# Optimization experiments

Hardware: AMD Instinct MI355X
Metric: run time of the kernel (lower is better)

Reference implementation:

```python
import jax, jax.numpy as jnp
import numpy as np

B, S, D_IN, H, D_OUT = 128, 2048, 256, 256, 256
FORECAST = 1

def setup_inputs() -> dict:
    key = jax.random.key(0)
    ks = jax.random.split(key, 20)
    def lin(k, o, i):
        bound = 1.0 / np.sqrt(i)
        return jax.random.uniform(k, (o, i), jnp.float32, -bound, bound)
    def bias(k, o, i):
        bound = 1.0 / np.sqrt(i)
        return jax.random.uniform(k, (o,), jnp.float32, -bound, bound)
    inp = {
        "x": jax.random.normal(ks[0], (B, S, D_IN), jnp.float32),
        # layer 0 (input_size -> hidden)
        "Wf0": lin(ks[1], H, D_IN), "bf0": bias(ks[2], H, D_IN), "Uf0": lin(ks[3], H, H),
        "Wi0": lin(ks[4], H, D_IN), "bi0": bias(ks[5], H, D_IN), "Ui0": lin(ks[6], H, H),
        "Wx0": lin(ks[7], H, D_IN), "bx0": bias(ks[8], H, D_IN),
        # layer 1 (hidden -> hidden)
        "Wf1": lin(ks[9], H, H), "bf1": bias(ks[10], H, H), "Uf1": lin(ks[11], H, H),
        "Wi1": lin(ks[12], H, H), "bi1": bias(ks[13], H, H), "Ui1": lin(ks[14], H, H),
        "Wx1": lin(ks[15], H, H), "bx1": bias(ks[16], H, H),
        # output head
        "fcW": lin(ks[17], D_OUT, H), "fcb": bias(ks[18], D_OUT, H),
    }
    return inp

def _ran_layer(xseq, Wf, bf, Uf, Wi, bi, Ui, Wx, bx):
    # xseq: [B, S, D]. Precompute all input projections in three batched GEMMs,
    # then scan only the recurrent part (h @ U.T + gates + elementwise update).
    xf = jnp.einsum('bsd,hd->bsh', xseq, Wf) + bf  # [B,S,H]
    xi = jnp.einsum('bsd,hd->bsh', xseq, Wi) + bi
    xp = jnp.einsum('bsd,hd->bsh', xseq, Wx) + bx
    def step(h, inp):
        xf_t, xi_t, xp_t = inp                      # each [B,H]
        f = jax.nn.sigmoid(xf_t + h @ Uf.T)
        i = jax.nn.sigmoid(xi_t + h @ Ui.T)
        h = f * h + i * xp_t
        return h, h
    h0 = jnp.zeros((xseq.shape[0], Uf.shape[0]), xseq.dtype)
    seq = (jnp.swapaxes(xf, 0, 1), jnp.swapaxes(xi, 0, 1), jnp.swapaxes(xp, 0, 1))
    _, hs = jax.lax.scan(step, h0, seq)             # hs: [S,B,H]
    return jnp.swapaxes(hs, 0, 1)                   # [B,S,H]

def reference(x, Wf0, bf0, Uf0, Wi0, bi0, Ui0, Wx0, bx0,
              Wf1, bf1, Uf1, Wi1, bi1, Ui1, Wx1, bx1, fcW, fcb):
    h1 = _ran_layer(x,  Wf0, bf0, Uf0, Wi0, bi0, Ui0, Wx0, bx0)
    h2 = _ran_layer(h1, Wf1, bf1, Uf1, Wi1, bi1, Ui1, Wx1, bx1)
    # dropout in eval mode == identity; take last FORECAST steps then fc
    out = h2[:, -FORECAST:, :]                      # [B,FORECAST,H]
    return jnp.einsum('bth,oh->bto', out, fcW) + fcb
```

## Files before the change

kernel.cpp:

```cpp
#include <hip/hip_runtime.h>
#include <hip/hip_bf16.h>
#include <cstdint>
#include <cstddef>


typedef __bf16 bf16;
typedef __bf16 bf16x8 __attribute__((ext_vector_type(8)));
typedef __bf16 bf16x4 __attribute__((ext_vector_type(4)));
typedef __bf16 bf16x2 __attribute__((ext_vector_type(2)));
typedef float  floatx4 __attribute__((ext_vector_type(4)));

#define B_   128
#define S_   2048
#define H_   256
#define NEG_LOG2E -1.442695040888963f
#define NGB  96
#define SMEM_BYTES (84 * 1024)

__global__ void prep_weights(
    const float* __restrict__ Wf0, const float* __restrict__ Wi0, const float* __restrict__ Wx0,
    const float* __restrict__ Wf1, const float* __restrict__ Wi1, const float* __restrict__ Wx1,
    const float* __restrict__ Uf0, const float* __restrict__ Ui0,
    const float* __restrict__ Uf1, const float* __restrict__ Ui1,
    const float* __restrict__ bf0, const float* __restrict__ bi0, const float* __restrict__ bx0,
    const float* __restrict__ bf1, const float* __restrict__ bi1, const float* __restrict__ bx1,
    const float* __restrict__ fcW,
    bf16* __restrict__ W0cat, bf16* __restrict__ W1cat,
    bf16* __restrict__ U0cat, bf16* __restrict__ U1cat,
    float* __restrict__ b0cat, float* __restrict__ b1cat, float* __restrict__ fcWT)
{
    int tid = blockIdx.x * blockDim.x + threadIdx.x;
    int nth = gridDim.x * blockDim.x;
    for (int idx = tid; idx < 768 * 256; idx += nth) {
        int r = idx >> 8, k = idx & 255, rr = r & 255;
        const float* s0 = (r < 256) ? Wf0 : ((r < 512) ? Wi0 : Wx0);
        const float* s1 = (r < 256) ? Wf1 : ((r < 512) ? Wi1 : Wx1);
        W0cat[idx] = (bf16)s0[rr * 256 + k];
        W1cat[idx] = (bf16)s1[rr * 256 + k];
    }
    for (int idx = tid; idx < 512 * 256; idx += nth) {
        int r = idx >> 8, k = idx & 255, rr = r & 255;
        U0cat[idx] = (bf16)((r < 256 ? Uf0 : Ui0)[rr * 256 + k]);
        U1cat[idx] = (bf16)((r < 256 ? Uf1 : Ui1)[rr * 256 + k]);
    }
    for (int idx = tid; idx < 768; idx += nth) {
        const float* s0 = (idx < 256) ? bf0 : ((idx < 512) ? bi0 : bx0);
        const float* s1 = (idx < 256) ? bf1 : ((idx < 512) ? bi1 : bx1);
        b0cat[idx] = s0[idx & 255];
        b1cat[idx] = s1[idx & 255];
    }
    for (int idx = tid; idx < 256 * 256; idx += nth) {
        int h = idx >> 8, o = idx & 255;
        fcWT[idx] = fcW[o * 256 + h];
    }
}

__global__ void convert_x(const float* __restrict__ x, bf16* __restrict__ xa, int t0, int T)
{
    int tid = blockIdx.x * blockDim.x + threadIdx.x;
    int d4 = tid & 63;
    int b  = (tid >> 6) & 127;
    int t  = tid >> 13;
    if (t >= T) return;
    const float4* src = (const float4*)(x + ((size_t)b * S_ + t0 + t) * H_) + d4;
    float4 v = *src;
    bf16x4 o = { (bf16)v.x, (bf16)v.y, (bf16)v.z, (bf16)v.w };
    *((bf16x4*)(xa + ((size_t)t * B_ + b) * H_) + d4) = o;
}

__device__ __forceinline__ void gemm_tile(
    char* smem,
    const bf16* __restrict__ Abase,
    const bf16* __restrict__ W, const float* __restrict__ bias,
    float* __restrict__ preP, int t, int nb)
{
    bf16* At = (bf16*)smem;
    bf16* Bt = (bf16*)smem + 128 * 32;
    int n0 = nb * 128;
    int tid = threadIdx.x;
    int lane = tid & 63, wave = tid >> 6;
    int wm = (wave >> 2) * 64, wn = (wave & 3) * 32;
    int qm = lane & 15, qk = lane >> 4;
    floatx4 acc[4][2] = {};

    for (int k0 = 0; k0 < 256; k0 += 32) {
        {
            int c = tid, row = c >> 2, kc = c & 3;
            *(bf16x8*)(At + c * 8) = *(const bf16x8*)(Abase + (size_t)row * 256 + k0 + kc * 8);
            *(bf16x8*)(Bt + c * 8) = *(const bf16x8*)(W + (size_t)(n0 + row) * 256 + k0 + kc * 8);
        }
        __syncthreads();
        bf16x8 af[4], bfr[2];
#pragma unroll
        for (int i = 0; i < 4; ++i)
            af[i] = *(const bf16x8*)(At + (wm + i * 16 + qm) * 32 + qk * 8);
#pragma unroll
        for (int n = 0; n < 2; ++n)
            bfr[n] = *(const bf16x8*)(Bt + (wn + n * 16 + qm) * 32 + qk * 8);
#pragma unroll
        for (int mi = 0; mi < 4; ++mi)
#pragma unroll
            for (int ni = 0; ni < 2; ++ni)
                acc[mi][ni] = __builtin_amdgcn_mfma_f32_16x16x32_bf16(af[mi], bfr[ni], acc[mi][ni], 0, 0, 0);
        __syncthreads();
    }
#pragma unroll
    for (int mi = 0; mi < 4; ++mi) {
        int b = wm + mi * 16 + qk * 4;
        int wgA = b >> 1;
#pragma unroll
        for (int ni = 0; ni < 2; ++ni) {
            int c = n0 + wn + ni * 16 + qm;
            int g = c >> 8;
            float bb = bias[c];
            float v0 = acc[mi][ni][0] + bb, v1 = acc[mi][ni][1] + bb;
            float v2 = acc[mi][ni][2] + bb, v3 = acc[mi][ni][3] + bb;
            if (g < 2) {
                v0 *= NEG_LOG2E; v1 *= NEG_LOG2E;
                v2 *= NEG_LOG2E; v3 *= NEG_LOG2E;
            }
            float2 w0 = { v0, v1 }, w1 = { v2, v3 };
            *(float2*)(preP + ((size_t)t * 64 + wgA)     * 1536 + (size_t)c * 2) = w0;
            *(float2*)(preP + ((size_t)t * 64 + wgA + 1) * 1536 + (size_t)c * 2) = w1;
        }
    }
}

__device__ __forceinline__ void rec_wg(
    char* smem, int wg,
    const float* __restrict__ preP,
    bf16* __restrict__ hout,
    const bf16* __restrict__ Ucat,
    float* __restrict__ hstate,
    int T)
{
    bf16* hbb = (bf16*)smem;
    const int tid = threadIdx.x, lane = tid & 63, wave = tid >> 6;
    const int qm = lane & 15, qk = lane >> 4;
    const int row = qk & 1;
    const int ch  = qk >> 1;
    const int cb  = wave * 32;
    const int col = cb + ch * 16 + qm;
    const int bbase = wg * 2;
    const bool selrow = (lane & 16) != 0;
    const bool selch  = (lane & 32) != 0;

    bf16x8 Ufr[2][8], Uir[2][8];
#pragma unroll
    for (int nt = 0; nt < 2; ++nt)
#pragma unroll
        for (int kt = 0; kt < 8; ++kt) {
            Ufr[nt][kt] = *(const bf16x8*)(Ucat + (size_t)(cb + nt * 16 + qm) * 256 + kt * 32 + qk * 8);
            Uir[nt][kt] = *(const bf16x8*)(Ucat + (size_t)(256 + cb + nt * 16 + qm) * 256 + kt * 32 + qk * 8);
        }
    {
        int r2 = tid >> 8, c2 = tid & 255;
        hbb[r2 * 272 + c2] = (bf16)hstate[(size_t)(bbase + r2) * 256 + c2];
    }
    float hm = hstate[(size_t)(bbase + row) * 256 + col];
    __syncthreads();

    const float* pw = preP + (size_t)wg * 1536 + (size_t)(col * 2 + row);
#define PLD(dst, tt) { size_t o_ = (size_t)(tt) * 98304;                   \
        dst[0] = pw[o_]; dst[1] = pw[o_ + 512]; dst[2] = pw[o_ + 1024]; }

    int cur = 0;

    auto pick = [&](floatx4 v0, floatx4 v1) -> float {
        float a0 = selrow ? v0[1] : v0[0];
        float a1 = selrow ? v1[1] : v1[0];
        return selch ? a1 : a0;
    };

    auto step = [&](int t, const float* p) {
        floatx4 f0{}, f1{}, i0{}, i1{};
        const bf16* hc = hbb + cur * (2 * 272);
#pragma unroll
        for (int kt = 0; kt < 8; ++kt) {
            bf16x8 a = *(const bf16x8*)(hc + (qm & 1) * 272 + kt * 32 + qk * 8);
            f0 = __builtin_amdgcn_mfma_f32_16x16x32_bf16(a, Ufr[0][kt], f0, 0, 0, 0);
            f1 = __builtin_amdgcn_mfma_f32_16x16x32_bf16(a, Ufr[1][kt], f1, 0, 0, 0);
            i0 = __builtin_amdgcn_mfma_f32_16x16x32_bf16(a, Uir[0][kt], i0, 0, 0, 0);
            i1 = __builtin_amdgcn_mfma_f32_16x16x32_bf16(a, Uir[1][kt], i1, 0, 0, 0);
        }
        float zf = pick(f0, f1), zi = pick(i0, i1);
        bf16* hn = hbb + (cur ^ 1) * (2 * 272);
        float ef = fminf(fmaf(zf, NEG_LOG2E, p[0]), 80.0f);
        float ei = fminf(fmaf(zi, NEG_LOG2E, p[1]), 80.0f);
        float A1 = 1.0f + __builtin_amdgcn_exp2f(ef);
        float B1 = 1.0f + __builtin_amdgcn_exp2f(ei);
        float N  = fmaf(hm, B1, p[2] * A1);
        hm = N * __builtin_amdgcn_rcpf(A1 * B1);
        hn[row * 272 + col] = (bf16)hm;
        asm volatile("s_waitcnt lgkmcnt(0)\n\ts_barrier" ::: "memory");
        if (hout) {
            int r2 = tid >> 8, c2 = tid & 255;
            hout[((size_t)t * 128 + bbase + r2) * 256 + c2] = hn[r2 * 272 + c2];
        }
        cur ^= 1;
    };

    float bA[3], bB[3], bC[3], bD[3];
    PLD(bA, 0);
    PLD(bB, 1);
    for (int t = 0; t < T; t += 4) {
        PLD(bC, (t + 2 < T) ? t + 2 : T - 1);
        step(t, bA);
        PLD(bD, (t + 3 < T) ? t + 3 : T - 1);
        step(t + 1, bB);
        PLD(bA, (t + 4 < T) ? t + 4 : T - 1);
        step(t + 2, bC);
        PLD(bB, (t + 5 < T) ? t + 5 : T - 1);
        step(t + 3, bD);
    }
#undef PLD
    hstate[(size_t)(bbase + row) * 256 + col] = hm;
}

__global__ __launch_bounds__(512) void mega(
    const bf16* __restrict__ xa, int t0n,
    const bf16* __restrict__ W0, const float* __restrict__ b0,
    const bf16* __restrict__ W1, const float* __restrict__ b1,
    const bf16* __restrict__ U0, const bf16* __restrict__ U1,
    float* __restrict__ h0s, float* __restrict__ h1s,
    float* __restrict__ pre0n,
    const float* __restrict__ pre0c,
    bf16*  __restrict__ h1bc,
    const bf16* __restrict__ h1bp,
    float* __restrict__ pre1p,
    const float* __restrict__ pre1pp,
    int flags, int T)
{
    __shared__ __align__(16) char smem[SMEM_BYTES];
    int bx = blockIdx.x;
    if (bx < 64) {
        if (flags & 1) rec_wg(smem, bx, pre0c, h1bc, U0, h0s, T);
        return;
    }
    if (bx < 128) {
        if (flags & 4) rec_wg(smem, bx - 64, pre1pp, nullptr, U1, h1s, T);
        return;
    }
    int ng0 = (flags & 8) ? T * 6 : 0;
    int ng1 = (flags & 2) ? T * 6 : 0;
    for (int tile = bx - 128; tile < ng0 + ng1; tile += NGB) {
        bool is0 = tile < ng0;
        int tt = is0 ? tile : tile - ng0;
        int t = tt / 6, nb = tt - t * 6;
        const bf16* A = is0 ? (xa + (size_t)(t0n + t) * 32768)
                            : (h1bp + (size_t)t * 32768);
        gemm_tile(smem, A, is0 ? W0 : W1, is0 ? b0 : b1,
                  is0 ? pre0n : pre1p, t, nb);
    }
}

__global__ void fc_head(const float* __restrict__ h2, const float* __restrict__ fcWT,
                        const float* __restrict__ fcb, float* __restrict__ out)
{
    int b = blockIdx.x, o = threadIdx.x;
    __shared__ float hrow[256];
    hrow[o] = h2[(size_t)b * 256 + o];
    __syncthreads();
    float acc = fcb[o];
#pragma unroll 8
    for (int h = 0; h < 256; ++h)
        acc = fmaf(hrow[h], fcWT[h * 256 + o], acc);
    out[(size_t)b * 256 + o] = acc;
}

extern "C" void kernel_launch(void* const* d_in, const int* in_sizes, int n_in,
                              void* d_out, int out_size, void* d_ws, size_t ws_size,
                              hipStream_t stream)
{
    (void)in_sizes; (void)n_in; (void)out_size;
    const float* x   = (const float*)d_in[0];
    const float* Wf0 = (const float*)d_in[1];
    const float* bf0 = (const float*)d_in[2];
    const float* Uf0 = (const float*)d_in[3];
    const float* Wi0 = (const float*)d_in[4];
    const float* bi0 = (const float*)d_in[5];
    const float* Ui0 = (const float*)d_in[6];
    const float* Wx0 = (const float*)d_in[7];
    const float* bx0 = (const float*)d_in[8];
    const float* Wf1 = (const float*)d_in[9];
    const float* bf1 = (const float*)d_in[10];
    const float* Uf1 = (const float*)d_in[11];
    const float* Wi1 = (const float*)d_in[12];
    const float* bi1 = (const float*)d_in[13];
    const float* Ui1 = (const float*)d_in[14];
    const float* Wx1 = (const float*)d_in[15];
    const float* bx1 = (const float*)d_in[16];
    const float* fcW = (const float*)d_in[17];
    const float* fcb = (const float*)d_in[18];

    char* p = (char*)d_ws;
    auto alloc = [&](size_t bytes) -> char* {
        char* r = p; p += (bytes + 255) & ~(size_t)255; return r;
    };
    bf16*  W0cat = (bf16*)alloc(768 * 256 * 2);
    bf16*  W1cat = (bf16*)alloc(768 * 256 * 2);
    bf16*  U0cat = (bf16*)alloc(512 * 256 * 2);
    bf16*  U1cat = (bf16*)alloc(512 * 256 * 2);
    float* b0cat = (float*)alloc(768 * 4);
    float* b1cat = (float*)alloc(768 * 4);
    float* fcWT  = (float*)alloc(256 * 256 * 4);
    float* h0s   = (float*)alloc(128 * 256 * 4);
    float* h1s   = (float*)alloc(128 * 256 * 4);
    size_t fixed = (size_t)(p - (char*)d_ws);

    int T_c = 128;
    while (T_c > 32 &&
           fixed + 134217728ULL + (size_t)T_c * 1703936ULL + 4096 > ws_size)
        T_c >>= 1;
    bf16*  xa    = (bf16*)alloc((size_t)S_ * 128 * 256 * 2);
    float* pre0s[2], *pre1s[2];
    bf16*  h1bs[2];
    pre0s[0] = (float*)alloc((size_t)T_c * 128 * 768 * 4);
    pre0s[1] = (float*)alloc((size_t)T_c * 128 * 768 * 4);
    pre1s[0] = (float*)alloc((size_t)T_c * 128 * 768 * 4);
    pre1s[1] = (float*)alloc((size_t)T_c * 128 * 768 * 4);
    h1bs[0]  = (bf16*)alloc((size_t)T_c * 128 * 256 * 2);
    h1bs[1]  = (bf16*)alloc((size_t)T_c * 128 * 256 * 2);

    hipMemsetAsync(h0s, 0, 128 * 256 * 4, stream);
    hipMemsetAsync(h1s, 0, 128 * 256 * 4, stream);

    prep_weights<<<512, 256, 0, stream>>>(Wf0, Wi0, Wx0, Wf1, Wi1, Wx1,
                                          Uf0, Ui0, Uf1, Ui1,
                                          bf0, bi0, bx0, bf1, bi1, bx1, fcW,
                                          W0cat, W1cat, U0cat, U1cat, b0cat, b1cat, fcWT);
    convert_x<<<S_ * 32, 256, 0, stream>>>(x, xa, 0, S_);

    int NC = S_ / T_c;
    for (int k = -1; k <= NC + 1; ++k) {
        int flags = 0;
        if (k >= 0 && k < NC)     flags |= 1;
        if (k >= 1 && k <= NC)    flags |= 2;
        if (k >= 2 && k <= NC+1)  flags |= 4;
        if (k <= NC - 2)          flags |= 8;
        mega<<<128 + NGB, 512, 0, stream>>>(
            xa, (k + 1) * T_c,
            W0cat, b0cat, W1cat, b1cat, U0cat, U1cat, h0s, h1s,
            pre0s[(k + 1) & 1],
            pre0s[k & 1],
            h1bs[k & 1],
            h1bs[(k - 1) & 1],
            pre1s[(k - 1) & 1],
            pre1s[k & 1],
            flags, T_c);
    }
    fc_head<<<128, 256, 0, stream>>>(h1s, fcWT, fcb, (float*)d_out);
}
```

Baseline: 2.329 ms.

## Process 16 batch rows per recurrent workgroup and free CUs for GEMM

Each recurrent workgroup now handles 16 batch rows instead of 2, so the MFMA tiles are fully used rather than mostly wasted, and each layer runs on 8 workgroups instead of 64. The freed CUs go to the input-projection GEMM pool (NGB raised from 96 to 208). The GEMM epilogue writes preactivations in a new layout matching the MFMA output fragment, so the recurrence loads them as float4. The cost is eight times more elementwise gate work per lane on the serial critical path, and the step barrier becomes a full __syncthreads.

```diff
diff --git a/kernel.cpp b/kernel.cpp
--- a/kernel.cpp
+++ b/kernel.cpp
@@ -14,7 +14,7 @@
 #define S_   2048
 #define H_   256
 #define NEG_LOG2E -1.442695040888963f
-#define NGB  96
+#define NGB  208
 #define SMEM_BYTES (84 * 1024)
 
 __global__ void prep_weights(
@@ -107,21 +107,22 @@
 #pragma unroll
     for (int mi = 0; mi < 4; ++mi) {
         int b = wm + mi * 16 + qk * 4;
-        int wgA = b >> 1;
+        int wgi = b >> 4, qk2 = (b >> 2) & 3;
 #pragma unroll
         for (int ni = 0; ni < 2; ++ni) {
             int c = n0 + wn + ni * 16 + qm;
-            int g = c >> 8;
+            int g = c >> 8, ch = c & 255, wv = ch >> 5, nt = (ch >> 4) & 1;
             float bb = bias[c];
-            float v0 = acc[mi][ni][0] + bb, v1 = acc[mi][ni][1] + bb;
-            float v2 = acc[mi][ni][2] + bb, v3 = acc[mi][ni][3] + bb;
-            if (g < 2) {
-                v0 *= NEG_LOG2E; v1 *= NEG_LOG2E;
-                v2 *= NEG_LOG2E; v3 *= NEG_LOG2E;
+            floatx4 v;
+#pragma unroll
+            for (int r = 0; r < 4; ++r) {
+                float val = acc[mi][ni][r] + bb;
+                v[r] = (g < 2) ? NEG_LOG2E * val : val;
             }
-            float2 w0 = { v0, v1 }, w1 = { v2, v3 };
-            *(float2*)(preP + ((size_t)t * 64 + wgA)     * 1536 + (size_t)c * 2) = w0;
-            *(float2*)(preP + ((size_t)t * 64 + wgA + 1) * 1536 + (size_t)c * 2) = w1;
+            size_t off = (size_t)t * 98304
+                       + (size_t)((wgi * 8 + wv) * 6 + g * 2 + nt) * 256
+                       + (size_t)(qk2 * 64 + qm * 4);
+            *(floatx4*)(preP + off) = v;
         }
     }
 }
@@ -134,16 +135,11 @@
     float* __restrict__ hstate,
     int T)
 {
-    bf16* hbb = (bf16*)smem;
+    bf16* hb0 = (bf16*)smem;
+    bf16* hb1 = (bf16*)smem + 16 * 264;
     const int tid = threadIdx.x, lane = tid & 63, wave = tid >> 6;
     const int qm = lane & 15, qk = lane >> 4;
-    const int row = qk & 1;
-    const int ch  = qk >> 1;
-    const int cb  = wave * 32;
-    const int col = cb + ch * 16 + qm;
-    const int bbase = wg * 2;
-    const bool selrow = (lane & 16) != 0;
-    const bool selch  = (lane & 32) != 0;
+    const int bbase = wg * 16, cb = wave * 32;
 
     bf16x8 Ufr[2][8], Uir[2][8];
 #pragma unroll
@@ -154,67 +150,79 @@
             Uir[nt][kt] = *(const bf16x8*)(Ucat + (size_t)(256 + cb + nt * 16 + qm) * 256 + kt * 32 + qk * 8);
         }
     {
-        int r2 = tid >> 8, c2 = tid & 255;
-        hbb[r2 * 272 + c2] = (bf16)hstate[(size_t)(bbase + r2) * 256 + c2];
-    }
-    float hm = hstate[(size_t)(bbase + row) * 256 + col];
+        int row = tid >> 5, c8 = (tid & 31) * 8;
+        const float* hs = hstate + (size_t)(bbase + row) * 256 + c8;
+        bf16x8 v;
+#pragma unroll
+        for (int j = 0; j < 8; ++j) v[j] = (bf16)hs[j];
+        *(bf16x8*)(hb0 + row * 264 + c8) = v;
+    }
+    float hm[2][4];
+#pragma unroll
+    for (int nt = 0; nt < 2; ++nt)
+#pragma unroll
+        for (int r = 0; r < 4; ++r)
+            hm[nt][r] = hstate[(size_t)(bbase + qk * 4 + r) * 256 + cb + nt * 16 + qm];
     __syncthreads();
 
-    const float* pw = preP + (size_t)wg * 1536 + (size_t)(col * 2 + row);
-#define PLD(dst, tt) { size_t o_ = (size_t)(tt) * 98304;                   \
-        dst[0] = pw[o_]; dst[1] = pw[o_ + 512]; dst[2] = pw[o_ + 1024]; }
-
+    const float4* pw = (const float4*)preP + (size_t)(wg * 8 + wave) * 384 + lane;
+#define PLD(dst, tt) { size_t o_ = (size_t)(tt) * 24576;                        \
+        dst[0] = pw[o_];       dst[1] = pw[o_ + 64];  dst[2] = pw[o_ + 128];    \
+        dst[3] = pw[o_ + 192]; dst[4] = pw[o_ + 256]; dst[5] = pw[o_ + 320]; }
+
+    float4 bufA[6], bufB[6];
+    PLD(bufA, 0);
     int cur = 0;
 
-    auto pick = [&](floatx4 v0, floatx4 v1) -> float {
-        float a0 = selrow ? v0[1] : v0[0];
-        float a1 = selrow ? v1[1] : v1[0];
-        return selch ? a1 : a0;
+    auto step = [&](int t, int curb, const float4* p) {
+        floatx4 accf[2] = {}, acci[2] = {};
+        const bf16* hc = curb ? hb1 : hb0;
+#pragma unroll
+        for (int kt = 0; kt < 8; ++kt) {
+            bf16x8 a = *(const bf16x8*)(hc + qm * 264 + kt * 32 + qk * 8);
+            accf[0] = __builtin_amdgcn_mfma_f32_16x16x32_bf16(a, Ufr[0][kt], accf[0], 0, 0, 0);
+            accf[1] = __builtin_amdgcn_mfma_f32_16x16x32_bf16(a, Ufr[1][kt], accf[1], 0, 0, 0);
+            acci[0] = __builtin_amdgcn_mfma_f32_16x16x32_bf16(a, Uir[0][kt], acci[0], 0, 0, 0);
+            acci[1] = __builtin_amdgcn_mfma_f32_16x16x32_bf16(a, Uir[1][kt], acci[1], 0, 0, 0);
+        }
+        bf16* hn = curb ? hb0 : hb1;
+#pragma unroll
+        for (int nt = 0; nt < 2; ++nt)
+#pragma unroll
+            for (int r = 0; r < 4; ++r) {
+                float pf = ((const float*)&p[nt])[r];
+                float pi = ((const float*)&p[2 + nt])[r];
+                float px = ((const float*)&p[4 + nt])[r];
+                float ef = fminf(fmaf(accf[nt][r], NEG_LOG2E, pf), 80.0f);
+                float ei = fminf(fmaf(acci[nt][r], NEG_LOG2E, pi), 80.0f);
+                float A1 = 1.0f + __builtin_amdgcn_exp2f(ef);
+                float B1 = 1.0f + __builtin_amdgcn_exp2f(ei);
+                float N  = fmaf(hm[nt][r], B1, px * A1);
+                float h  = N * __builtin_amdgcn_rcpf(A1 * B1);
+                hm[nt][r] = h;
+                hn[(qk * 4 + r) * 264 + cb + nt * 16 + qm] = (bf16)h;
+            }
+        __syncthreads();
+        if (hout) {
+            int row = tid >> 5, c8 = (tid & 31) * 8;
+            bf16x8 v = *(const bf16x8*)(hn + row * 264 + c8);
+            *(bf16x8*)(hout + ((size_t)t * 128 + bbase + row) * 256 + c8) = v;
+        }
     };
 
-    auto step = [&](int t, const float* p) {
-        floatx4 f0{}, f1{}, i0{}, i1{};
-        const bf16* hc = hbb + cur * (2 * 272);
-#pragma unroll
-        for (int kt = 0; kt < 8; ++kt) {
-            bf16x8 a = *(const bf16x8*)(hc + (qm & 1) * 272 + kt * 32 + qk * 8);
-            f0 = __builtin_amdgcn_mfma_f32_16x16x32_bf16(a, Ufr[0][kt], f0, 0, 0, 0);
-            f1 = __builtin_amdgcn_mfma_f32_16x16x32_bf16(a, Ufr[1][kt], f1, 0, 0, 0);
-            i0 = __builtin_amdgcn_mfma_f32_16x16x32_bf16(a, Uir[0][kt], i0, 0, 0, 0);
-            i1 = __builtin_amdgcn_mfma_f32_16x16x32_bf16(a, Uir[1][kt], i1, 0, 0, 0);
-        }
-        float zf = pick(f0, f1), zi = pick(i0, i1);
-        bf16* hn = hbb + (cur ^ 1) * (2 * 272);
-        float ef = fminf(fmaf(zf, NEG_LOG2E, p[0]), 80.0f);
-        float ei = fminf(fmaf(zi, NEG_LOG2E, p[1]), 80.0f);
-        float A1 = 1.0f + __builtin_amdgcn_exp2f(ef);
-        float B1 = 1.0f + __builtin_amdgcn_exp2f(ei);
-        float N  = fmaf(hm, B1, p[2] * A1);
-        hm = N * __builtin_amdgcn_rcpf(A1 * B1);
-        hn[row * 272 + col] = (bf16)hm;
-        asm volatile("s_waitcnt lgkmcnt(0)\n\ts_barrier" ::: "memory");
-        if (hout) {
-            int r2 = tid >> 8, c2 = tid & 255;
-            hout[((size_t)t * 128 + bbase + r2) * 256 + c2] = hn[r2 * 272 + c2];
-        }
-        cur ^= 1;
-    };
-
-    float bA[3], bB[3], bC[3], bD[3];
-    PLD(bA, 0);
-    PLD(bB, 1);
-    for (int t = 0; t < T; t += 4) {
-        PLD(bC, (t + 2 < T) ? t + 2 : T - 1);
-        step(t, bA);
-        PLD(bD, (t + 3 < T) ? t + 3 : T - 1);
-        step(t + 1, bB);
-        PLD(bA, (t + 4 < T) ? t + 4 : T - 1);
-        step(t + 2, bC);
-        PLD(bB, (t + 5 < T) ? t + 5 : T - 1);
-        step(t + 3, bD);
+    for (int t = 0; t < T; t += 2) {
+        PLD(bufB, t + 1);
+        step(t, cur, bufA);  cur ^= 1;
+        int t2 = (t + 2 < T) ? t + 2 : t;
+        PLD(bufA, t2);
+        step(t + 1, cur, bufB); cur ^= 1;
     }
 #undef PLD
-    hstate[(size_t)(bbase + row) * 256 + col] = hm;
+#pragma unroll
+    for (int nt = 0; nt < 2; ++nt)
+#pragma unroll
+        for (int r = 0; r < 4; ++r)
+            hstate[(size_t)(bbase + qk * 4 + r) * 256 + cb + nt * 16 + qm] = hm[nt][r];
 }
 
 __global__ __launch_bounds__(512) void mega(
@@ -233,17 +241,17 @@
 {
     __shared__ __align__(16) char smem[SMEM_BYTES];
     int bx = blockIdx.x;
-    if (bx < 64) {
+    if (bx < 8) {
         if (flags & 1) rec_wg(smem, bx, pre0c, h1bc, U0, h0s, T);
         return;
     }
-    if (bx < 128) {
-        if (flags & 4) rec_wg(smem, bx - 64, pre1pp, nullptr, U1, h1s, T);
+    if (bx < 16) {
+        if (flags & 4) rec_wg(smem, bx - 8, pre1pp, nullptr, U1, h1s, T);
         return;
     }
     int ng0 = (flags & 8) ? T * 6 : 0;
     int ng1 = (flags & 2) ? T * 6 : 0;
-    for (int tile = bx - 128; tile < ng0 + ng1; tile += NGB) {
+    for (int tile = bx - 16; tile < ng0 + ng1; tile += NGB) {
         bool is0 = tile < ng0;
         int tt = is0 ? tile : tile - ng0;
         int t = tt / 6, nb = tt - t * 6;
@@ -338,7 +346,7 @@
         if (k >= 1 && k <= NC)    flags |= 2;
         if (k >= 2 && k <= NC+1)  flags |= 4;
         if (k <= NC - 2)          flags |= 8;
-        mega<<<128 + NGB, 512, 0, stream>>>(
+        mega<<<16 + NGB, 512, 0, stream>>>(
             xa, (k + 1) * T_c,
             W0cat, b0cat, W1cat, b1cat, U0cat, U1cat, h0s, h1s,
             pre0s[(k + 1) & 1],
```

Measured after the change: 2.912 ms. +25.0%, slower.
